# Kernel optimization log

Measured on AMD Instinct MI355X. Metric: run time of the kernel, lower is better.

## Reference

```python
import jax, jax.numpy as jnp
import numpy as np


def setup_inputs() -> dict:
    key = jax.random.key(0)
    k1, k2, k3, k4, k5 = jax.random.split(key, 5)
    B_, S, D_in, D_out, R = 2, 2048, 4096, 4096, 4
    return {
        "x": jax.random.normal(k1, (B_, S, D_in), dtype=jnp.float32),
        "weight": jax.random.normal(k2, (D_out, D_in), dtype=jnp.float32) * 0.02,
        "bias": jax.random.normal(k3, (D_out,), dtype=jnp.float32) * 0.02,
        "scale_A": jax.random.normal(k4, (D_out, R), dtype=jnp.float32),
        "scale_B": jax.random.normal(k5, (R, D_in), dtype=jnp.float32),
        "rank_magnitude": jnp.ones((R,), dtype=jnp.float32),
    }


def reference(x, weight, bias, scale_A, scale_B, rank_magnitude):
    # Factored forward with default bound_mode='tanh', A_max=B_max=1.0, pad=0:
    #   y = sum_k g_k * A[:, k] * ((x * B[k]) @ Q.T) + bias
    Q = weight  # snapped_mode=None, _Q=None -> Q = raw weight
    A = jnp.tanh(scale_A)            # [O, R]
    Bm = jnp.tanh(scale_B)           # [R, I] (pad == 0)
    Ag = A * rank_magnitude[None, :]  # fold g_k into A -> [O, R]
    # [b,s,i] x [r,i] -> [b,s,r,i]; contract i with Q [o,i]; weight by Ag [o,r]
    y = jnp.einsum("bsi,ri,oi,or->bso", x, Bm, Q, Ag)
    return y + bias
```

## Files before the change

### kernel.cpp

```cpp
#include <hip/hip_runtime.h>
#include <hip/hip_bf16.h>

typedef __attribute__((ext_vector_type(8))) short bf16x8;
typedef __attribute__((ext_vector_type(4))) float f32x4;
typedef __attribute__((ext_vector_type(4))) short s16x4;

#define M_DIM 4096
#define N_DIM 4096
#define K_DIM 4096
#define R_DIM 4

__device__ __forceinline__ short to_bf16(float f) {
    __hip_bfloat16 h = __float2bfloat16(f);
    return *reinterpret_cast<short*>(&h);
}

__global__ __launch_bounds__(256)
void k_prep(const float* __restrict__ sA, const float* __restrict__ sB,
            const float* __restrict__ g, float* __restrict__ tB,
            float* __restrict__ tAg) {
    int i = blockIdx.x * 256 + threadIdx.x;
    if (i < R_DIM * K_DIM) {
        tB[i] = tanhf(sB[i]);
    } else {
        int j = i - R_DIM * K_DIM;
        tAg[j] = tanhf(sA[j]) * g[j & 3];
    }
}

__global__ __launch_bounds__(256)
void k_xcast(const float* __restrict__ x, __hip_bfloat16* __restrict__ xb) {
    const size_t i = ((size_t)blockIdx.x * 256 + threadIdx.x) << 3;
    float4 u = *(const float4*)&x[i];
    float4 v = *(const float4*)&x[i + 4];
    bf16x8 pk;
    pk[0] = to_bf16(u.x); pk[1] = to_bf16(u.y);
    pk[2] = to_bf16(u.z); pk[3] = to_bf16(u.w);
    pk[4] = to_bf16(v.x); pk[5] = to_bf16(v.y);
    pk[6] = to_bf16(v.z); pk[7] = to_bf16(v.w);
    *(bf16x8*)&xb[i] = pk;
}

__global__ __launch_bounds__(256)
void k_weff(const float* __restrict__ w, const float* __restrict__ tB,
            const float* __restrict__ tAg, __hip_bfloat16* __restrict__ weff) {
    const int o = blockIdx.x;
    const float a0 = tAg[o * 4 + 0];
    const float a1 = tAg[o * 4 + 1];
    const float a2 = tAg[o * 4 + 2];
    const float a3 = tAg[o * 4 + 3];
#pragma unroll
    for (int it = 0; it < 4; ++it) {
        const int i = (it * 256 + (int)threadIdx.x) << 2;
        float4 wv = *(const float4*)&w[(size_t)o * K_DIM + i];
        float4 b0 = *(const float4*)&tB[0 * K_DIM + i];
        float4 b1 = *(const float4*)&tB[1 * K_DIM + i];
        float4 b2 = *(const float4*)&tB[2 * K_DIM + i];
        float4 b3 = *(const float4*)&tB[3 * K_DIM + i];
        float s0 = a0 * b0.x + a1 * b1.x + a2 * b2.x + a3 * b3.x;
        float s1 = a0 * b0.y + a1 * b1.y + a2 * b2.y + a3 * b3.y;
        float s2 = a0 * b0.z + a1 * b1.z + a2 * b2.z + a3 * b3.z;
        float s3 = a0 * b0.w + a1 * b1.w + a2 * b2.w + a3 * b3.w;
        s16x4 pk;
        pk[0] = to_bf16(wv.x * s0);
        pk[1] = to_bf16(wv.y * s1);
        pk[2] = to_bf16(wv.z * s2);
        pk[3] = to_bf16(wv.w * s3);
        *(s16x4*)&weff[(size_t)o * K_DIM + i] = pk;
    }
}

#define MFMA(A, B, C) __builtin_amdgcn_mfma_f32_16x16x32_bf16(A, B, C, 0, 0, 0)

#define RD_A(d, q) \
    a0 = *(const bf16x8*)(LA0 + (d)*32768 + (q)*4096); \
    a1 = *(const bf16x8*)(LA1 + (d)*32768 + (q)*4096); \
    a2 = *(const bf16x8*)(LA0 + (d)*32768 + (q)*4096 + 2048); \
    a3 = *(const bf16x8*)(LA1 + (d)*32768 + (q)*4096 + 2048);

#define RD_B(d) \
    b0 = *(const bf16x8*)(LB0 + (d)*32768 + 0); \
    b1 = *(const bf16x8*)(LB1 + (d)*32768 + 0); \
    b2 = *(const bf16x8*)(LB0 + (d)*32768 + 2048); \
    b3 = *(const bf16x8*)(LB1 + (d)*32768 + 2048); \
    b4 = *(const bf16x8*)(LB0 + (d)*32768 + 4096); \
    b5 = *(const bf16x8*)(LB1 + (d)*32768 + 4096); \
    b6 = *(const bf16x8*)(LB0 + (d)*32768 + 6144); \
    b7 = *(const bf16x8*)(LB1 + (d)*32768 + 6144);

#define VM2 asm volatile("s_waitcnt vmcnt(2)" ::: "memory")

#define PH(d, q, READS_STMT, STAGE_STMT, VM_STMT) \
    { READS_STMT; \
      STAGE_STMT; \
      VM_STMT; \
      __builtin_amdgcn_s_barrier(); \
      asm volatile("s_waitcnt lgkmcnt(0)" ::: "memory"); \
      __builtin_amdgcn_sched_barrier(0); \
      __builtin_amdgcn_s_setprio(1); \
       \
      acc[2*(q)][0]   = MFMA(a0, b0, acc[2*(q)][0]); \
      acc[2*(q)][1]   = MFMA(a0, b2, acc[2*(q)][1]); \
      acc[2*(q)][2]   = MFMA(a0, b4, acc[2*(q)][2]); \
      acc[2*(q)][3]   = MFMA(a0, b6, acc[2*(q)][3]); \
      acc[2*(q)+1][0] = MFMA(a2, b0, acc[2*(q)+1][0]); \
      acc[2*(q)+1][1] = MFMA(a2, b2, acc[2*(q)+1][1]); \
      acc[2*(q)+1][2] = MFMA(a2, b4, acc[2*(q)+1][2]); \
      acc[2*(q)+1][3] = MFMA(a2, b6, acc[2*(q)+1][3]); \
       \
      acc[2*(q)][0]   = MFMA(a1, b1, acc[2*(q)][0]); \
      acc[2*(q)][1]   = MFMA(a1, b3, acc[2*(q)][1]); \
      acc[2*(q)][2]   = MFMA(a1, b5, acc[2*(q)][2]); \
      acc[2*(q)][3]   = MFMA(a1, b7, acc[2*(q)][3]); \
      acc[2*(q)+1][0] = MFMA(a3, b1, acc[2*(q)+1][0]); \
      acc[2*(q)+1][1] = MFMA(a3, b3, acc[2*(q)+1][1]); \
      acc[2*(q)+1][2] = MFMA(a3, b5, acc[2*(q)+1][2]); \
      acc[2*(q)+1][3] = MFMA(a3, b7, acc[2*(q)+1][3]); \
      __builtin_amdgcn_s_setprio(0); }

__global__ __launch_bounds__(512)
void k_gemm8(const __hip_bfloat16* __restrict__ xb,
             const __hip_bfloat16* __restrict__ weff,
             const float* __restrict__ bias, float* __restrict__ out) {
    __shared__ short lds[65536];

    const int tid  = threadIdx.x;
    const int lane = tid & 63;
    const int wid  = tid >> 6;
    const int wr   = wid >> 2;
    const int wc   = wid & 3;
    const int l15  = lane & 15;
    const int cb0  = (lane >> 4) << 4;

    const int bid = blockIdx.x;
    const int swz = (bid & 7) * 32 + (bid >> 3);
    const int m0g = (swz >> 4) << 8;
    const int n0g = (swz & 15) << 8;

    const int mask = (l15 & 7) << 4;
    const int cbs0 = cb0 ^ mask;
    const int cbs1 = (cb0 + 64) ^ mask;
    const char* LAb = (const char*)lds + wr * 16384 + l15 * 128;
    const char* LA0 = LAb + cbs0;
    const char* LA1 = LAb + cbs1;
    const char* LBb = (const char*)lds + 65536 + (wc >> 1) * 16384 +
                      ((wc & 1) * 64 + l15) * 128;
    const char* LB0 = LBb + cbs0;
    const char* LB1 = LBb + cbs1;

    const int rowL  = tid >> 3;
    const int colbL = ((tid * 16) & 127) ^ ((rowL & 7) << 4);
    const __hip_bfloat16* gA = xb   + ((size_t)(m0g + rowL) << 12) + (colbL >> 1);
    const __hip_bfloat16* gB = weff + ((size_t)(n0g + rowL) << 12) + (colbL >> 1);

    auto STG = [&](const __hip_bfloat16* gbase, int k0, int dstShort) {
        __builtin_amdgcn_global_load_lds(
            (const __attribute__((address_space(1))) void*)(gbase + k0),
            (__attribute__((address_space(3))) void*)&lds[dstShort + tid * 8],
            16, 0, 0);
        __builtin_amdgcn_global_load_lds(
            (const __attribute__((address_space(1))) void*)(gbase + 262144 + k0),
            (__attribute__((address_space(3))) void*)&lds[dstShort + 4096 + tid * 8],
            16, 0, 0);
    };

    f32x4 acc[8][4] = {};
    bf16x8 a0, a1, a2, a3, b0, b1, b2, b3, b4, b5, b6, b7;

    STG(gB,          0,  32768);
    STG(gB + 524288, 0,  40960);
    STG(gA,          0,  0);
    STG(gA + 524288, 0,  8192);
    STG(gB,          64, 49152);
    VM2;
    __builtin_amdgcn_s_barrier();
    __builtin_amdgcn_sched_barrier(0);

    for (int i = 0; i < 32; ++i) {
        const int t1k = (2 * i + 1) * 64;
        const int kA  = (2 * i + 2 < 64 ? 2 * i + 2 : 63) * 64;
        const int kB  = (2 * i + 3 < 64 ? 2 * i + 3 : 63) * 64;

        PH(0, 0, RD_A(0, 0); RD_B(0), STG(gB + 524288, t1k, 57344), );
        PH(0, 1, RD_A(0, 1),          STG(gA,          t1k, 16384), );
        PH(0, 2, RD_A(0, 2),          STG(gA + 524288, t1k, 24576), );
        PH(0, 3, RD_A(0, 3),          STG(gB,          kA,  32768), VM2);
        PH(1, 0, RD_A(1, 0); RD_B(1), STG(gB + 524288, kA,  40960), );
        PH(1, 1, RD_A(1, 1),          STG(gA,          kA,  0), );
        PH(1, 2, RD_A(1, 2),          STG(gA + 524288, kA,  8192), );
        PH(1, 3, RD_A(1, 3),          STG(gB,          kB,  49152), VM2);
    }

#pragma unroll
    for (int n = 0; n < 4; ++n) {
        const int col = n0g + wc * 64 + n * 16 + l15;
        const float bv = bias[col];
#pragma unroll
        for (int m = 0; m < 8; ++m) {
            const int rbase = m0g + wr * 128 + m * 16 + ((lane >> 4) << 2);
#pragma unroll
            for (int j = 0; j < 4; ++j)
                out[(size_t)(rbase + j) * N_DIM + col] = acc[m][n][j] + bv;
        }
    }
}

extern "C" void kernel_launch(void* const* d_in, const int* in_sizes, int n_in,
                              void* d_out, int out_size, void* d_ws, size_t ws_size,
                              hipStream_t stream) {
    const float* x    = (const float*)d_in[0];
    const float* w    = (const float*)d_in[1];
    const float* bias = (const float*)d_in[2];
    const float* sA   = (const float*)d_in[3];
    const float* sB   = (const float*)d_in[4];
    const float* g    = (const float*)d_in[5];
    float* out = (float*)d_out;

    __hip_bfloat16* weff = (__hip_bfloat16*)d_ws;
    __hip_bfloat16* xb   = (__hip_bfloat16*)((char*)d_ws + (32ull << 20));
    float* tB  = (float*)((char*)d_ws + (64ull << 20));
    float* tAg = (float*)((char*)d_ws + (64ull << 20) + (R_DIM * K_DIM * 4));

    k_prep<<<dim3((2 * R_DIM * K_DIM) / 256), dim3(256), 0, stream>>>(sA, sB, g, tB, tAg);
    k_xcast<<<dim3((M_DIM * K_DIM) / (256 * 8)), dim3(256), 0, stream>>>(x, xb);
    k_weff<<<dim3(N_DIM), dim3(256), 0, stream>>>(w, tB, tAg, weff);
    k_gemm8<<<dim3((M_DIM / 256) * (N_DIM / 256)), dim3(512), 0, stream>>>(xb, weff, bias, out);
}
```

Baseline: 154.0 us.

## Restructure GEMM main loop into triple-buffered A with 32-MFMA phases

Reorganizes the bf16 GEMM K-loop so that A tiles rotate through three LDS buffers while B stays double-buffered. Each phase now reads eight A fragments and issues 32 MFMAs, where before it read four and issued 16, so there are half as many barriers per K step. Global-to-LDS staging moves whole 4-chunk tiles at once, waited on with vmcnt(4). LDS grows to 160KB and launch_bounds requests two blocks per CU. The risks are that LDS demand may allow only one block per CU, and that the more complex rotation adds register pressure from the extra fragments.

```diff
diff --git a/kernel.cpp b/kernel.cpp
--- a/kernel.cpp
+++ b/kernel.cpp
@@ -72,25 +72,70 @@
 
 #define MFMA(A, B, C) __builtin_amdgcn_mfma_f32_16x16x32_bf16(A, B, C, 0, 0, 0)
 
-#define RD_A(d, q) \
-    a0 = *(const bf16x8*)(LA0 + (d)*32768 + (q)*4096); \
-    a1 = *(const bf16x8*)(LA1 + (d)*32768 + (q)*4096); \
-    a2 = *(const bf16x8*)(LA0 + (d)*32768 + (q)*4096 + 2048); \
-    a3 = *(const bf16x8*)(LA1 + (d)*32768 + (q)*4096 + 2048);
-
-#define RD_B(d) \
-    b0 = *(const bf16x8*)(LB0 + (d)*32768 + 0); \
-    b1 = *(const bf16x8*)(LB1 + (d)*32768 + 0); \
-    b2 = *(const bf16x8*)(LB0 + (d)*32768 + 2048); \
-    b3 = *(const bf16x8*)(LB1 + (d)*32768 + 2048); \
-    b4 = *(const bf16x8*)(LB0 + (d)*32768 + 4096); \
-    b5 = *(const bf16x8*)(LB1 + (d)*32768 + 4096); \
-    b6 = *(const bf16x8*)(LB0 + (d)*32768 + 6144); \
-    b7 = *(const bf16x8*)(LB1 + (d)*32768 + 6144);
-
-#define VM2 asm volatile("s_waitcnt vmcnt(2)" ::: "memory")
-
-#define PH(d, q, READS_STMT, STAGE_STMT, VM_STMT) \
+#define RA0 0
+#define RA1 32768
+#define RA2 65536
+#define SA0 0
+#define SA1 16384
+#define SA2 32768
+#define SB0 49152
+#define SB1 65536
+
+#define RD_A8(ab, qq) \
+    aA = *(const bf16x8*)(LA0 + (ab) + (qq)*4096 + 0); \
+    aB = *(const bf16x8*)(LA1 + (ab) + (qq)*4096 + 0); \
+    aC = *(const bf16x8*)(LA0 + (ab) + (qq)*4096 + 2048); \
+    aD = *(const bf16x8*)(LA1 + (ab) + (qq)*4096 + 2048); \
+    aE = *(const bf16x8*)(LA0 + (ab) + (qq)*4096 + 4096); \
+    aF = *(const bf16x8*)(LA1 + (ab) + (qq)*4096 + 4096); \
+    aG = *(const bf16x8*)(LA0 + (ab) + (qq)*4096 + 6144); \
+    aH = *(const bf16x8*)(LA1 + (ab) + (qq)*4096 + 6144);
+
+#define RD_B8(bb) \
+    b0 = *(const bf16x8*)(LB0 + (bb) + 0);    b1 = *(const bf16x8*)(LB1 + (bb) + 0); \
+    b2 = *(const bf16x8*)(LB0 + (bb) + 2048); b3 = *(const bf16x8*)(LB1 + (bb) + 2048); \
+    b4 = *(const bf16x8*)(LB0 + (bb) + 4096); b5 = *(const bf16x8*)(LB1 + (bb) + 4096); \
+    b6 = *(const bf16x8*)(LB0 + (bb) + 6144); b7 = *(const bf16x8*)(LB1 + (bb) + 6144);
+
+#define MFMA32(qq) \
+     \
+    acc[2*(qq)+0][0] = MFMA(aA, b0, acc[2*(qq)+0][0]); \
+    acc[2*(qq)+0][1] = MFMA(aA, b2, acc[2*(qq)+0][1]); \
+    acc[2*(qq)+0][2] = MFMA(aA, b4, acc[2*(qq)+0][2]); \
+    acc[2*(qq)+0][3] = MFMA(aA, b6, acc[2*(qq)+0][3]); \
+    acc[2*(qq)+1][0] = MFMA(aC, b0, acc[2*(qq)+1][0]); \
+    acc[2*(qq)+1][1] = MFMA(aC, b2, acc[2*(qq)+1][1]); \
+    acc[2*(qq)+1][2] = MFMA(aC, b4, acc[2*(qq)+1][2]); \
+    acc[2*(qq)+1][3] = MFMA(aC, b6, acc[2*(qq)+1][3]); \
+    acc[2*(qq)+2][0] = MFMA(aE, b0, acc[2*(qq)+2][0]); \
+    acc[2*(qq)+2][1] = MFMA(aE, b2, acc[2*(qq)+2][1]); \
+    acc[2*(qq)+2][2] = MFMA(aE, b4, acc[2*(qq)+2][2]); \
+    acc[2*(qq)+2][3] = MFMA(aE, b6, acc[2*(qq)+2][3]); \
+    acc[2*(qq)+3][0] = MFMA(aG, b0, acc[2*(qq)+3][0]); \
+    acc[2*(qq)+3][1] = MFMA(aG, b2, acc[2*(qq)+3][1]); \
+    acc[2*(qq)+3][2] = MFMA(aG, b4, acc[2*(qq)+3][2]); \
+    acc[2*(qq)+3][3] = MFMA(aG, b6, acc[2*(qq)+3][3]); \
+     \
+    acc[2*(qq)+0][0] = MFMA(aB, b1, acc[2*(qq)+0][0]); \
+    acc[2*(qq)+0][1] = MFMA(aB, b3, acc[2*(qq)+0][1]); \
+    acc[2*(qq)+0][2] = MFMA(aB, b5, acc[2*(qq)+0][2]); \
+    acc[2*(qq)+0][3] = MFMA(aB, b7, acc[2*(qq)+0][3]); \
+    acc[2*(qq)+1][0] = MFMA(aD, b1, acc[2*(qq)+1][0]); \
+    acc[2*(qq)+1][1] = MFMA(aD, b3, acc[2*(qq)+1][1]); \
+    acc[2*(qq)+1][2] = MFMA(aD, b5, acc[2*(qq)+1][2]); \
+    acc[2*(qq)+1][3] = MFMA(aD, b7, acc[2*(qq)+1][3]); \
+    acc[2*(qq)+2][0] = MFMA(aF, b1, acc[2*(qq)+2][0]); \
+    acc[2*(qq)+2][1] = MFMA(aF, b3, acc[2*(qq)+2][1]); \
+    acc[2*(qq)+2][2] = MFMA(aF, b5, acc[2*(qq)+2][2]); \
+    acc[2*(qq)+2][3] = MFMA(aF, b7, acc[2*(qq)+2][3]); \
+    acc[2*(qq)+3][0] = MFMA(aH, b1, acc[2*(qq)+3][0]); \
+    acc[2*(qq)+3][1] = MFMA(aH, b3, acc[2*(qq)+3][1]); \
+    acc[2*(qq)+3][2] = MFMA(aH, b5, acc[2*(qq)+3][2]); \
+    acc[2*(qq)+3][3] = MFMA(aH, b7, acc[2*(qq)+3][3]);
+
+#define VM4 asm volatile("s_waitcnt vmcnt(4)" ::: "memory")
+
+#define PH4(READS_STMT, STAGE_STMT, VM_STMT, qq) \
     { READS_STMT; \
       STAGE_STMT; \
       VM_STMT; \
@@ -98,31 +143,20 @@
       asm volatile("s_waitcnt lgkmcnt(0)" ::: "memory"); \
       __builtin_amdgcn_sched_barrier(0); \
       __builtin_amdgcn_s_setprio(1); \
-       \
-      acc[2*(q)][0]   = MFMA(a0, b0, acc[2*(q)][0]); \
-      acc[2*(q)][1]   = MFMA(a0, b2, acc[2*(q)][1]); \
-      acc[2*(q)][2]   = MFMA(a0, b4, acc[2*(q)][2]); \
-      acc[2*(q)][3]   = MFMA(a0, b6, acc[2*(q)][3]); \
-      acc[2*(q)+1][0] = MFMA(a2, b0, acc[2*(q)+1][0]); \
-      acc[2*(q)+1][1] = MFMA(a2, b2, acc[2*(q)+1][1]); \
-      acc[2*(q)+1][2] = MFMA(a2, b4, acc[2*(q)+1][2]); \
-      acc[2*(q)+1][3] = MFMA(a2, b6, acc[2*(q)+1][3]); \
-       \
-      acc[2*(q)][0]   = MFMA(a1, b1, acc[2*(q)][0]); \
-      acc[2*(q)][1]   = MFMA(a1, b3, acc[2*(q)][1]); \
-      acc[2*(q)][2]   = MFMA(a1, b5, acc[2*(q)][2]); \
-      acc[2*(q)][3]   = MFMA(a1, b7, acc[2*(q)][3]); \
-      acc[2*(q)+1][0] = MFMA(a3, b1, acc[2*(q)+1][0]); \
-      acc[2*(q)+1][1] = MFMA(a3, b3, acc[2*(q)+1][1]); \
-      acc[2*(q)+1][2] = MFMA(a3, b5, acc[2*(q)+1][2]); \
-      acc[2*(q)+1][3] = MFMA(a3, b7, acc[2*(q)+1][3]); \
+      MFMA32(qq); \
       __builtin_amdgcn_s_setprio(0); }
 
-__global__ __launch_bounds__(512)
+#define ITER4(RAu, RAv, SAu, SAw, KT1, KT2, KT3) \
+    PH4(RD_A8(RAu, 0); RD_B8(0),     STGT(gB, KT1, SB1), , 0) \
+    PH4(RD_A8(RAu, 2),               STGT(gA, KT2, SAw), VM4, 2) \
+    PH4(RD_A8(RAv, 0); RD_B8(32768), STGT(gB, KT2, SB0), , 0) \
+    PH4(RD_A8(RAv, 2),               STGT(gA, KT3, SAu), VM4, 2)
+
+__global__ __launch_bounds__(512, 2)
 void k_gemm8(const __hip_bfloat16* __restrict__ xb,
              const __hip_bfloat16* __restrict__ weff,
              const float* __restrict__ bias, float* __restrict__ out) {
-    __shared__ short lds[65536];
+    __shared__ short lds[81920];
 
     const int tid  = threadIdx.x;
     const int lane = tid & 63;
@@ -143,7 +177,7 @@
     const char* LAb = (const char*)lds + wr * 16384 + l15 * 128;
     const char* LA0 = LAb + cbs0;
     const char* LA1 = LAb + cbs1;
-    const char* LBb = (const char*)lds + 65536 + (wc >> 1) * 16384 +
+    const char* LBb = (const char*)lds + 98304 + (wc >> 1) * 16384 +
                       ((wc & 1) * 64 + l15) * 128;
     const char* LB0 = LBb + cbs0;
     const char* LB1 = LBb + cbs1;
@@ -153,43 +187,35 @@
     const __hip_bfloat16* gA = xb   + ((size_t)(m0g + rowL) << 12) + (colbL >> 1);
     const __hip_bfloat16* gB = weff + ((size_t)(n0g + rowL) << 12) + (colbL >> 1);
 
-    auto STG = [&](const __hip_bfloat16* gbase, int k0, int dstShort) {
-        __builtin_amdgcn_global_load_lds(
-            (const __attribute__((address_space(1))) void*)(gbase + k0),
-            (__attribute__((address_space(3))) void*)&lds[dstShort + tid * 8],
-            16, 0, 0);
-        __builtin_amdgcn_global_load_lds(
-            (const __attribute__((address_space(1))) void*)(gbase + 262144 + k0),
-            (__attribute__((address_space(3))) void*)&lds[dstShort + 4096 + tid * 8],
-            16, 0, 0);
+    auto STGT = [&](const __hip_bfloat16* gbase, int k0, int dstShort) {
+#pragma unroll
+        for (int p = 0; p < 4; ++p) {
+            __builtin_amdgcn_global_load_lds(
+                (const __attribute__((address_space(1))) void*)(gbase + p * 262144 + k0),
+                (__attribute__((address_space(3))) void*)&lds[dstShort + p * 4096 + tid * 8],
+                16, 0, 0);
+        }
     };
 
     f32x4 acc[8][4] = {};
-    bf16x8 a0, a1, a2, a3, b0, b1, b2, b3, b4, b5, b6, b7;
-
-    STG(gB,          0,  32768);
-    STG(gB + 524288, 0,  40960);
-    STG(gA,          0,  0);
-    STG(gA + 524288, 0,  8192);
-    STG(gB,          64, 49152);
-    VM2;
+    bf16x8 aA, aB, aC, aD, aE, aF, aG, aH;
+    bf16x8 b0, b1, b2, b3, b4, b5, b6, b7;
+
+    STGT(gB, 0, SB0);
+    STGT(gA, 0, SA0);
+    STGT(gA, 64, SA1);
+    asm volatile("s_waitcnt vmcnt(0)" ::: "memory");
     __builtin_amdgcn_s_barrier();
     __builtin_amdgcn_sched_barrier(0);
 
-    for (int i = 0; i < 32; ++i) {
-        const int t1k = (2 * i + 1) * 64;
-        const int kA  = (2 * i + 2 < 64 ? 2 * i + 2 : 63) * 64;
-        const int kB  = (2 * i + 3 < 64 ? 2 * i + 3 : 63) * 64;
-
-        PH(0, 0, RD_A(0, 0); RD_B(0), STG(gB + 524288, t1k, 57344), );
-        PH(0, 1, RD_A(0, 1),          STG(gA,          t1k, 16384), );
-        PH(0, 2, RD_A(0, 2),          STG(gA + 524288, t1k, 24576), );
-        PH(0, 3, RD_A(0, 3),          STG(gB,          kA,  32768), VM2);
-        PH(1, 0, RD_A(1, 0); RD_B(1), STG(gB + 524288, kA,  40960), );
-        PH(1, 1, RD_A(1, 1),          STG(gA,          kA,  0), );
-        PH(1, 2, RD_A(1, 2),          STG(gA + 524288, kA,  8192), );
-        PH(1, 3, RD_A(1, 3),          STG(gB,          kB,  49152), VM2);
-    }
+    for (int j = 0; j < 10; ++j) {
+        const int t = 6 * j;
+        ITER4(RA0, RA1, SA0, SA2, (t + 1) * 64, (t + 2) * 64, (t + 3) * 64);
+        ITER4(RA2, RA0, SA2, SA1, (t + 3) * 64, (t + 4) * 64, (t + 5) * 64);
+        ITER4(RA1, RA2, SA1, SA0, (t + 5) * 64, (t + 6) * 64, (t + 7) * 64);
+    }
+    ITER4(RA0, RA1, SA0, SA2, 61 * 64, 62 * 64, 63 * 64);
+    ITER4(RA2, RA0, SA2, SA1, 63 * 64, 63 * 64, 63 * 64);
 
 #pragma unroll
     for (int n = 0; n < 4; ++n) {
@@ -199,8 +225,8 @@
         for (int m = 0; m < 8; ++m) {
             const int rbase = m0g + wr * 128 + m * 16 + ((lane >> 4) << 2);
 #pragma unroll
-            for (int j = 0; j < 4; ++j)
-                out[(size_t)(rbase + j) * N_DIM + col] = acc[m][n][j] + bv;
+            for (int j2 = 0; j2 < 4; ++j2)
+                out[(size_t)(rbase + j2) * N_DIM + col] = acc[m][n][j2] + bv;
         }
     }
 }
```

Measured after the change: 152.2 us. Within noise of the previous version (-1.2%).
